# Kernel tuning notes

Measured on AMD Instinct MI355X. Metric: run time of the kernel, lower is better.

The kernel has to match this reference:

```python
import jax, jax.numpy as jnp
import numpy as np

# The torch module's per-item while-loop repeatedly does masked argmin + mask
# update. That greedy extraction is mathematically a stable sort of the valid
# (unmasked) entries by time (stable argsort reproduces argmin's lowest-index
# tie-breaking), with positions past the valid count filled with pad_value.

def setup_inputs() -> dict:
    key = jax.random.key(0)
    k1, k2 = jax.random.split(key)
    B, L = 4096, 2048
    time = jax.random.uniform(k1, (B, L), dtype=jnp.float32)
    mask = jax.random.randint(k2, (B, L), 0, 2).astype(jnp.bool_)  # True = already visited / excluded
    pad_value = L  # sentinel index used to pad unpredicted slots
    return {"time": time, "mask": mask, "pad_value": pad_value}


def reference(time, mask, pad_value):
    # time: [B, L] float32, mask: [B, L] bool (True = excluded)
    B, L = time.shape
    # Masked entries pushed past every valid entry (original uses 1e6 fill,
    # but masked entries are never emitted since the loop stops at msk.all();
    # +inf preserves that invariant for the sorted formulation).
    keys = jnp.where(mask, jnp.inf, time)
    order = jnp.argsort(keys, axis=-1)               # stable: ties -> lowest index, same as argmin
    valid = jnp.sum(~mask, axis=-1)                  # [B] number of emitted indices per item
    pos = jnp.arange(L, dtype=valid.dtype)[None, :]  # [1, L]
    pred = jnp.where(pos < valid[:, None], order, pad_value)  # [B, L]
    return pred.astype(jnp.int32), valid.astype(jnp.int32)
```

## Files before the change

kernel.cpp:

```cpp
#include <hip/hip_runtime.h>
#include <stdint.h>

#define LROW 2048
#define THREADS 256
#define NBINS 2048

__global__ __launch_bounds__(THREADS) void time_greedy_bucket_kernel(
    const float* __restrict__ time,
    const int* __restrict__ mask,
    const int* __restrict__ pad_value_p,
    int* __restrict__ pred,
    int* __restrict__ valid_out)
{
    __shared__ uint64_t keys[LROW];
    __shared__ uint32_t hist[NBINS];
    __shared__ uint32_t wsum[4];

    const int row = blockIdx.x;
    const int tid = threadIdx.x;
    const int lane = tid & 63;
    const int wid = tid >> 6;

#pragma unroll
    for (int e = 0; e < NBINS / THREADS; ++e) {
        hist[tid + e * THREADS] = 0;
        keys[tid + e * THREADS] = ~0ull;
    }
    __syncthreads();

    const float4* trow4 = (const float4*)(time + (size_t)row * LROW);
    const int4*   mrow4 = (const int4*)(mask + (size_t)row * LROW);

    uint32_t ukey[8];
    int      bkt[8];
    int      mval[8];
#pragma unroll
    for (int c = 0; c < 2; ++c) {
        const int v = tid + c * THREADS;
        const float4 tq = trow4[v];
        const int4   mq = mrow4[v];
        const float tf[4] = {tq.x, tq.y, tq.z, tq.w};
        const int   mf[4] = {mq.x, mq.y, mq.z, mq.w};
#pragma unroll
        for (int j = 0; j < 4; ++j) {
            const int e = c * 4 + j;
            const uint32_t fb = __float_as_uint(tf[j]);
            ukey[e] = fb ^ ((uint32_t)((int32_t)fb >> 31) | 0x80000000u);
            int b = (int)(tf[j] * (float)NBINS);
            b = (b < 0) ? 0 : ((b > NBINS - 1) ? NBINS - 1 : b);
            bkt[e] = b;
            mval[e] = mf[j];
            if (!mf[j]) atomicAdd(&hist[b], 1u);
        }
    }
    __syncthreads();

    uint32_t h[8];
    uint32_t lsum = 0;
#pragma unroll
    for (int e = 0; e < 8; ++e) {
        h[e] = hist[tid * 8 + e];
        lsum += h[e];
    }
    uint32_t incl = lsum;
#pragma unroll
    for (int off = 1; off < 64; off <<= 1) {
        const uint32_t y = __shfl_up(incl, off, 64);
        if (lane >= off) incl += y;
    }
    if (lane == 63) wsum[wid] = incl;
    __syncthreads();
    uint32_t woff = 0, total = 0;
#pragma unroll
    for (int w = 0; w < 4; ++w) {
        const uint32_t s = wsum[w];
        if (w < wid) woff += s;
        total += s;
    }
    uint32_t run = woff + incl - lsum;
#pragma unroll
    for (int e = 0; e < 8; ++e) {
        hist[tid * 8 + e] = run;
        run += h[e];
    }
    __syncthreads();

#pragma unroll
    for (int c = 0; c < 2; ++c) {
#pragma unroll
        for (int j = 0; j < 4; ++j) {
            const int e = c * 4 + j;
            if (!mval[e]) {
                const int i = 4 * tid + c * (4 * THREADS) + j;
                const uint32_t pos = atomicAdd(&hist[bkt[e]], 1u);
                keys[pos] = ((uint64_t)ukey[e] << 32) | (uint32_t)i;
            }
        }
    }
    __syncthreads();

#pragma unroll
    for (int q = 0; q < NBINS / THREADS; ++q) {
        const int b = tid * (NBINS / THREADS) + q;
        const uint32_t start = (b == 0) ? 0u : hist[b - 1];
        const uint32_t end = hist[b];
        for (uint32_t i = start + 1; i < end; ++i) {
            const uint64_t v = keys[i];
            uint32_t j = i;
            while (j > start && keys[j - 1] > v) {
                keys[j] = keys[j - 1];
                --j;
            }
            keys[j] = v;
        }
    }
    __syncthreads();

    const int vld = (int)total;
    const int pad = pad_value_p[0];
    int4* prow4 = (int4*)(pred + (size_t)row * LROW);
#pragma unroll
    for (int c = 0; c < 2; ++c) {
        const int v = tid + c * THREADS;
        const int base = 4 * v;
        int4 o;
        o.x = (base + 0 < vld) ? (int)(uint32_t)keys[base + 0] : pad;
        o.y = (base + 1 < vld) ? (int)(uint32_t)keys[base + 1] : pad;
        o.z = (base + 2 < vld) ? (int)(uint32_t)keys[base + 2] : pad;
        o.w = (base + 3 < vld) ? (int)(uint32_t)keys[base + 3] : pad;
        prow4[v] = o;
    }
    if (tid == 0) valid_out[row] = vld;
}

extern "C" void kernel_launch(void* const* d_in, const int* in_sizes, int n_in,
                              void* d_out, int out_size, void* d_ws, size_t ws_size,
                              hipStream_t stream) {
    const float* time = (const float*)d_in[0];
    const int* mask = (const int*)d_in[1];
    const int* pad_value = (const int*)d_in[2];

    const int B = in_sizes[0] / LROW;

    int* pred = (int*)d_out;
    int* valid_out = pred + (size_t)B * LROW;

    time_greedy_bucket_kernel<<<B, THREADS, 0, stream>>>(time, mask, pad_value,
                                                         pred, valid_out);
}
```

Measured before the change: 118.1 us.

## Halve bucket count, swizzle histogram layout, drop key init, use strided output stores

Cuts the bucket count to 1024 and stores the histogram in a swizzled layout so the per-thread prefix scan reads and writes are conflict-free in shared memory. The 2048-entry key initialisation is removed, since only positions below the valid count are read. The output write changes from int4 vector stores with 64-bit key reads to coalesced scalar stores. Fewer buckets means about two elements per bucket, so the per-bucket insertion sorts do slightly more work.

After: 113.7 us. 1.04x faster.

```diff
diff --git a/kernel.cpp b/kernel.cpp
--- a/kernel.cpp
+++ b/kernel.cpp
@@ -3,7 +3,12 @@
 
 #define LROW 2048
 #define THREADS 256
-#define NBINS 2048
+#define NBINS 1024
+#define BPT (NBINS / THREADS)
+
+__device__ __forceinline__ int swz(int b) {
+    return ((b & (BPT - 1)) << 8) + (b >> 2);
+}
 
 __global__ __launch_bounds__(THREADS) void time_greedy_bucket_kernel(
     const float* __restrict__ time,
@@ -22,10 +27,7 @@
     const int wid = tid >> 6;
 
 #pragma unroll
-    for (int e = 0; e < NBINS / THREADS; ++e) {
-        hist[tid + e * THREADS] = 0;
-        keys[tid + e * THREADS] = ~0ull;
-    }
+    for (int e = 0; e < BPT; ++e) hist[tid + e * THREADS] = 0;
     __syncthreads();
 
     const float4* trow4 = (const float4*)(time + (size_t)row * LROW);
@@ -50,16 +52,16 @@
             b = (b < 0) ? 0 : ((b > NBINS - 1) ? NBINS - 1 : b);
             bkt[e] = b;
             mval[e] = mf[j];
-            if (!mf[j]) atomicAdd(&hist[b], 1u);
+            if (!mf[j]) atomicAdd(&hist[swz(b)], 1u);
         }
     }
     __syncthreads();
 
-    uint32_t h[8];
+    uint32_t h[BPT];
     uint32_t lsum = 0;
 #pragma unroll
-    for (int e = 0; e < 8; ++e) {
-        h[e] = hist[tid * 8 + e];
+    for (int e = 0; e < BPT; ++e) {
+        h[e] = hist[e * THREADS + tid];
         lsum += h[e];
     }
     uint32_t incl = lsum;
@@ -79,8 +81,8 @@
     }
     uint32_t run = woff + incl - lsum;
 #pragma unroll
-    for (int e = 0; e < 8; ++e) {
-        hist[tid * 8 + e] = run;
+    for (int e = 0; e < BPT; ++e) {
+        hist[e * THREADS + tid] = run;
         run += h[e];
     }
     __syncthreads();
@@ -92,7 +94,7 @@
             const int e = c * 4 + j;
             if (!mval[e]) {
                 const int i = 4 * tid + c * (4 * THREADS) + j;
-                const uint32_t pos = atomicAdd(&hist[bkt[e]], 1u);
+                const uint32_t pos = atomicAdd(&hist[swz(bkt[e])], 1u);
                 keys[pos] = ((uint64_t)ukey[e] << 32) | (uint32_t)i;
             }
         }
@@ -100,10 +102,10 @@
     __syncthreads();
 
 #pragma unroll
-    for (int q = 0; q < NBINS / THREADS; ++q) {
-        const int b = tid * (NBINS / THREADS) + q;
-        const uint32_t start = (b == 0) ? 0u : hist[b - 1];
-        const uint32_t end = hist[b];
+    for (int e = 0; e < BPT; ++e) {
+        const int b = BPT * tid + e;
+        const uint32_t start = (b == 0) ? 0u : hist[swz(b - 1)];
+        const uint32_t end = hist[swz(b)];
         for (uint32_t i = start + 1; i < end; ++i) {
             const uint64_t v = keys[i];
             uint32_t j = i;
@@ -118,17 +120,12 @@
 
     const int vld = (int)total;
     const int pad = pad_value_p[0];
-    int4* prow4 = (int4*)(pred + (size_t)row * LROW);
+    int* prow = pred + (size_t)row * LROW;
 #pragma unroll
-    for (int c = 0; c < 2; ++c) {
-        const int v = tid + c * THREADS;
-        const int base = 4 * v;
-        int4 o;
-        o.x = (base + 0 < vld) ? (int)(uint32_t)keys[base + 0] : pad;
-        o.y = (base + 1 < vld) ? (int)(uint32_t)keys[base + 1] : pad;
-        o.z = (base + 2 < vld) ? (int)(uint32_t)keys[base + 2] : pad;
-        o.w = (base + 3 < vld) ? (int)(uint32_t)keys[base + 3] : pad;
-        prow4[v] = o;
+    for (int c = 0; c < LROW / THREADS; ++c) {
+        const int i = tid + c * THREADS;
+        const uint64_t k = keys[i];
+        prow[i] = (i < vld) ? (int)(uint32_t)k : pad;
     }
     if (tid == 0) valid_out[row] = vld;
 }
```
